# Performance work log

Hardware: AMD Instinct MI355X
Metric: run time of the kernel (lower is better)

## Reference

```python
import jax, jax.numpy as jnp
import numpy as np

M, K, N, G = 4096, 4096, 11008, 128


def setup_inputs() -> dict:
    key = jax.random.key(0)
    k1, k2, k3, k4, k5 = jax.random.split(key, 5)
    inp = jax.random.normal(k1, (M, K), dtype=jnp.float32)
    # int4 quantized weights, unpacked to one value per element, range [0, 16)
    qweight = jax.random.randint(k2, (K, N), 0, 16, dtype=jnp.int32)
    # group-wise scales / zero-points: one per (group along K, output column)
    scales = jax.random.uniform(k3, (K // G, N), dtype=jnp.float32, minval=0.001, maxval=0.02)
    qzeros = jax.random.randint(k4, (K // G, N), 0, 16, dtype=jnp.int32)
    bias = jax.random.normal(k5, (N,), dtype=jnp.float32) * 0.01
    return {"input": inp, "qweight": qweight, "scales": scales,
            "qzeros": qzeros, "bias": bias, "group_size": G}


def reference(input, qweight, scales, qzeros, bias, group_size):
    # Dequantize: w[k, n] = (q[k, n] - zp[k//G, n]) * scale[k//G, n]
    zp_full = jnp.repeat(qzeros.astype(jnp.float32), group_size, axis=0)   # [K, N]
    sc_full = jnp.repeat(scales, group_size, axis=0)                        # [K, N]
    w = (qweight.astype(jnp.float32) - zp_full) * sc_full                   # [K, N]
    # mm_bias_int4: out = input @ dequant(W) + bias
    return jnp.dot(input, w) + bias[None, :]
```

## Files before the change

kernel.cpp:

```cpp
#include <hip/hip_runtime.h>
#include <hip/hip_bf16.h>
#include <stdint.h>

#define MDIM 4096
#define KDIM 4096
#define NDIM 11008
#define NT   (KDIM / 32)

typedef __bf16 bf16x8 __attribute__((ext_vector_type(8)));
typedef float  f32x4  __attribute__((ext_vector_type(4)));

__global__ __launch_bounds__(512) void int4_gemm_mfma(
    const float* __restrict__ A, const int* __restrict__ Q,
    const float* __restrict__ S, const int* __restrict__ Z,
    const float* __restrict__ bias, float* __restrict__ out)
{
    __shared__ __bf16 sA[2][256 * 32];
    __shared__ __bf16 sB[2][256 * 32];

    auto SW = [](int row, int c) -> int {
        return ((row >> 1) << 7) + (((((row & 1) << 2) | c) ^ ((row >> 1) & 7)) << 4);
    };

    const int nbm = MDIM / 256;
    const int nwg = (MDIM / 256) * (NDIM / 256);
    const int xcd = blockIdx.x & 7;
    const int wg  = xcd * (nwg >> 3) + (blockIdx.x >> 3);
    const int bm  = wg % nbm;
    const int bn  = wg / nbm;
    const int m0 = bm * 256, n0 = bn * 256;

    const int t    = threadIdx.x;
    const int lane = t & 63;
    const int wave = t >> 6;
    const int wm   = (wave >> 2) * 128;
    const int wn   = (wave & 3) * 64;
    const int fr   = lane & 15;
    const int fq   = lane >> 4;

    const int arow = t >> 1;
    const int acb  = (t & 1) * 2;
    const int bn2  = (t & 127) * 2;
    const int bko  = (t >> 7) * 8;
    const int bcc  = t >> 7;

    f32x4 acc[8][4];
    #pragma unroll
    for (int i = 0; i < 8; ++i)
        #pragma unroll
        for (int j = 0; j < 4; ++j)
            #pragma unroll
            for (int r = 0; r < 4; ++r)
                acc[i][j][r] = 0.0f;

    const float* aP = A + (size_t)(m0 + arow) * KDIM + (t & 1) * 16;
    const int*   qP = Q + (size_t)bko * NDIM + n0 + bn2;

    float4 ra0, ra1, ra2, ra3;
    int2   rq[8];
    float2 sc;
    int2   zp;

    auto LOAD = [&](int kt) {
        ra0 = ((const float4*)aP)[0];
        ra1 = ((const float4*)aP)[1];
        ra2 = ((const float4*)aP)[2];
        ra3 = ((const float4*)aP)[3];
        const int* q = qP;
        #pragma unroll
        for (int j = 0; j < 8; ++j) {
            rq[j] = *(const int2*)q;
            q += NDIM;
        }
        if ((kt & 3) == 0) {
            const int g = kt >> 2;
            sc = *(const float2*)(S + (size_t)g * NDIM + n0 + bn2);
            zp = *(const int2*)  (Z + (size_t)g * NDIM + n0 + bn2);
        }
        aP += 32;
        qP += (size_t)32 * NDIM;
    };

    auto STORE = [&](int buf) {
        bf16x8 v0, v1;
        v0[0] = (__bf16)ra0.x; v0[1] = (__bf16)ra0.y;
        v0[2] = (__bf16)ra0.z; v0[3] = (__bf16)ra0.w;
        v0[4] = (__bf16)ra1.x; v0[5] = (__bf16)ra1.y;
        v0[6] = (__bf16)ra1.z; v0[7] = (__bf16)ra1.w;
        v1[0] = (__bf16)ra2.x; v1[1] = (__bf16)ra2.y;
        v1[2] = (__bf16)ra2.z; v1[3] = (__bf16)ra2.w;
        v1[4] = (__bf16)ra3.x; v1[5] = (__bf16)ra3.y;
        v1[6] = (__bf16)ra3.z; v1[7] = (__bf16)ra3.w;
        *(bf16x8*)((char*)sA[buf] + SW(arow, acb))     = v0;
        *(bf16x8*)((char*)sA[buf] + SW(arow, acb + 1)) = v1;

        const float zs0 = -(float)zp.x * sc.x;
        const float zs1 = -(float)zp.y * sc.y;
        bf16x8 w0, w1;
        #pragma unroll
        for (int j = 0; j < 8; ++j) {
            w0[j] = (__bf16)((float)rq[j].x * sc.x + zs0);
            w1[j] = (__bf16)((float)rq[j].y * sc.y + zs1);
        }
        *(bf16x8*)((char*)sB[buf] + SW(bn2,     bcc)) = w0;
        *(bf16x8*)((char*)sB[buf] + SW(bn2 + 1, bcc)) = w1;
    };

    auto FRAGS = [&](int buf, bf16x8 (&aF)[8], bf16x8 (&bF)[4]) {
        #pragma unroll
        for (int i = 0; i < 8; ++i)
            aF[i] = *(const bf16x8*)((char*)sA[buf] + SW(wm + 16 * i + fr, fq));
        #pragma unroll
        for (int j = 0; j < 4; ++j)
            bF[j] = *(const bf16x8*)((char*)sB[buf] + SW(wn + 16 * j + fr, fq));
    };

    auto MFMAS = [&](bf16x8 (&aF)[8], bf16x8 (&bF)[4]) {
        __builtin_amdgcn_s_setprio(1);
        #pragma unroll
        for (int i = 0; i < 8; ++i)
            #pragma unroll
            for (int j = 0; j < 4; ++j)
                acc[i][j] = __builtin_amdgcn_mfma_f32_16x16x32_bf16(
                                aF[i], bF[j], acc[i][j], 0, 0, 0);
        __builtin_amdgcn_s_setprio(0);
    };

    auto BAR = [&]() {
        asm volatile("s_waitcnt lgkmcnt(0)" ::: "memory");
        __builtin_amdgcn_s_barrier();
    };

    LOAD(0);
    STORE(0);
    LOAD(1);
    BAR();

    for (int kt = 0; kt < NT; kt += 2) {
        {
            bf16x8 aF[8], bF[4];
            FRAGS(0, aF, bF);
            STORE(1);
            if (kt + 2 < NT) LOAD(kt + 2);
            MFMAS(aF, bF);
            BAR();
        }
        {
            bf16x8 aF[8], bF[4];
            FRAGS(1, aF, bF);
            if (kt + 2 < NT) STORE(0);
            if (kt + 3 < NT) LOAD(kt + 3);
            MFMAS(aF, bF);
            BAR();
        }
    }

    float bj[4];
    #pragma unroll
    for (int j = 0; j < 4; ++j)
        bj[j] = bias[n0 + wn + 16 * j + fr];

    #pragma unroll
    for (int i = 0; i < 8; ++i) {
        #pragma unroll
        for (int r = 0; r < 4; ++r) {
            const int m = m0 + wm + 16 * i + fq * 4 + r;
            float* op = out + (size_t)m * NDIM + n0 + wn + fr;
            #pragma unroll
            for (int j = 0; j < 4; ++j)
                op[16 * j] = acc[i][j][r] + bj[j];
        }
    }
}

extern "C" void kernel_launch(void* const* d_in, const int* in_sizes, int n_in,
                              void* d_out, int out_size, void* d_ws, size_t ws_size,
                              hipStream_t stream) {
    const float* A    = (const float*)d_in[0];
    const int*   Q    = (const int*)d_in[1];
    const float* S    = (const float*)d_in[2];
    const int*   Z    = (const int*)d_in[3];
    const float* bias = (const float*)d_in[4];
    float* out = (float*)d_out;

    const int grid = (MDIM / 256) * (NDIM / 256);
    int4_gemm_mfma<<<dim3(grid), dim3(512), 0, stream>>>(A, Q, S, Z, bias, out);
}
```

Measured before the change: 895.3 us.

## Split each K-step into four barrier-separated phases interleaving LDS reads, stores and MFMAs

Restructures the main loop so each k-tile step runs as four phases of 8 MFMAs. Fragment loads, the A store, the B dequant-and-store and the global loads are spread across those phases, and sched_barrier plus s_barrier fence them apart. The aim is a ping-pong style schedule where waves overlap LDS and global traffic with matrix math instead of doing all memory work before one large MFMA block. The cost is extra workgroup barriers per step, which can add stall time if the waves fall out of lockstep.

```diff
diff --git a/kernel.cpp b/kernel.cpp
--- a/kernel.cpp
+++ b/kernel.cpp
@@ -81,7 +81,7 @@
         qP += (size_t)32 * NDIM;
     };
 
-    auto STORE = [&](int buf) {
+    auto STORE_A = [&](int buf) {
         bf16x8 v0, v1;
         v0[0] = (__bf16)ra0.x; v0[1] = (__bf16)ra0.y;
         v0[2] = (__bf16)ra0.z; v0[3] = (__bf16)ra0.w;
@@ -93,7 +93,9 @@
         v1[6] = (__bf16)ra3.z; v1[7] = (__bf16)ra3.w;
         *(bf16x8*)((char*)sA[buf] + SW(arow, acb))     = v0;
         *(bf16x8*)((char*)sA[buf] + SW(arow, acb + 1)) = v1;
-
+    };
+
+    auto STORE_B = [&](int buf) {
         const float zs0 = -(float)zp.x * sc.x;
         const float zs1 = -(float)zp.y * sc.y;
         bf16x8 w0, w1;
@@ -106,54 +108,81 @@
         *(bf16x8*)((char*)sB[buf] + SW(bn2 + 1, bcc)) = w1;
     };
 
-    auto FRAGS = [&](int buf, bf16x8 (&aF)[8], bf16x8 (&bF)[4]) {
-        #pragma unroll
-        for (int i = 0; i < 8; ++i)
-            aF[i] = *(const bf16x8*)((char*)sA[buf] + SW(wm + 16 * i + fr, fq));
-        #pragma unroll
-        for (int j = 0; j < 4; ++j)
-            bF[j] = *(const bf16x8*)((char*)sB[buf] + SW(wn + 16 * j + fr, fq));
-    };
-
-    auto MFMAS = [&](bf16x8 (&aF)[8], bf16x8 (&bF)[4]) {
-        __builtin_amdgcn_s_setprio(1);
-        #pragma unroll
-        for (int i = 0; i < 8; ++i)
-            #pragma unroll
-            for (int j = 0; j < 4; ++j)
-                acc[i][j] = __builtin_amdgcn_mfma_f32_16x16x32_bf16(
-                                aF[i], bF[j], acc[i][j], 0, 0, 0);
-        __builtin_amdgcn_s_setprio(0);
-    };
-
-    auto BAR = [&]() {
+    auto PH_WAIT = [&]() {
+        __builtin_amdgcn_sched_barrier(0);
+        __builtin_amdgcn_s_barrier();
         asm volatile("s_waitcnt lgkmcnt(0)" ::: "memory");
+        __builtin_amdgcn_sched_barrier(0);
+    };
+    auto PH_END = [&]() {
+        __builtin_amdgcn_sched_barrier(0);
         __builtin_amdgcn_s_barrier();
     };
 
+    #define MM8(I0, J0)                                                     \
+        do {                                                                \
+            __builtin_amdgcn_s_setprio(1);                                  \
+            _Pragma("unroll")                                               \
+            for (int i_ = 0; i_ < 4; ++i_)                                  \
+                _Pragma("unroll")                                           \
+                for (int j_ = 0; j_ < 2; ++j_)                              \
+                    acc[(I0) + i_][(J0) + j_] =                             \
+                        __builtin_amdgcn_mfma_f32_16x16x32_bf16(            \
+                            aF[(I0) + i_], bF[(J0) + j_],                   \
+                            acc[(I0) + i_][(J0) + j_], 0, 0, 0);            \
+            __builtin_amdgcn_s_setprio(0);                                  \
+        } while (0)
+
+    auto STEP = [&](int buf, int kstage, int kload) {
+        bf16x8 aF[8], bF[4];
+        const char* bA = (const char*)sA[buf];
+        const char* bB = (const char*)sB[buf];
+
+        #pragma unroll
+        for (int i = 0; i < 4; ++i)
+            aF[i] = *(const bf16x8*)(bA + SW(wm + 16 * i + fr, fq));
+        #pragma unroll
+        for (int j = 0; j < 2; ++j)
+            bF[j] = *(const bf16x8*)(bB + SW(wn + 16 * j + fr, fq));
+        PH_WAIT();
+        MM8(0, 0);
+        PH_END();
+
+        #pragma unroll
+        for (int i = 4; i < 8; ++i)
+            aF[i] = *(const bf16x8*)(bA + SW(wm + 16 * i + fr, fq));
+        #pragma unroll
+        for (int j = 2; j < 4; ++j)
+            bF[j] = *(const bf16x8*)(bB + SW(wn + 16 * j + fr, fq));
+        if (kstage < NT) STORE_A(buf ^ 1);
+        PH_WAIT();
+        MM8(0, 2);
+        PH_END();
+
+        if (kstage < NT) STORE_B(buf ^ 1);
+        if (kload < NT) LOAD(kload);
+        PH_WAIT();
+        MM8(4, 0);
+        PH_END();
+
+        MM8(4, 2);
+        __builtin_amdgcn_sched_barrier(0);
+        __builtin_amdgcn_s_barrier();
+    };
+
     LOAD(0);
-    STORE(0);
+    STORE_A(0);
+    STORE_B(0);
     LOAD(1);
-    BAR();
+    asm volatile("s_waitcnt lgkmcnt(0)" ::: "memory");
+    __builtin_amdgcn_s_barrier();
 
     for (int kt = 0; kt < NT; kt += 2) {
-        {
-            bf16x8 aF[8], bF[4];
-            FRAGS(0, aF, bF);
-            STORE(1);
-            if (kt + 2 < NT) LOAD(kt + 2);
-            MFMAS(aF, bF);
-            BAR();
-        }
-        {
-            bf16x8 aF[8], bF[4];
-            FRAGS(1, aF, bF);
-            if (kt + 2 < NT) STORE(0);
-            if (kt + 3 < NT) LOAD(kt + 3);
-            MFMAS(aF, bF);
-            BAR();
-        }
+        STEP(0, kt + 1, kt + 2);
+        STEP(1, kt + 2, kt + 3);
     }
+
+    #undef MM8
 
     float bj[4];
     #pragma unroll
```

Measured after the change: 981.8 us. 9.7% more time.
